# Optimization experiments

Measured on AMD Instinct MI355X. Metric: run time of the kernel, lower is better.

Reference implementation:

```python
import jax, jax.numpy as jnp
import numpy as np

B, T_CHAR, E, N_CHARS, T_TAG = 128, 256, 512, 128, 32


def _rn(k, shape, scale=1.0):
    return jax.random.normal(k, shape, dtype=jnp.float32) * scale


def setup_inputs() -> dict:
    key = jax.random.key(0)
    ks = jax.random.split(key, 24)
    W = 0.05  # param init scale
    tgt_idx = jax.random.randint(ks[4], (B, T_CHAR), 0, N_CHARS)
    return {
        "char_encoding": _rn(ks[0], (B, T_CHAR, E)),
        "char_hn": _rn(ks[1], (2, B, E // 2)),
        "char_cn": _rn(ks[2], (2, B, E // 2)),
        "tag_encoding": _rn(ks[3], (B, T_TAG, E)),
        "true_output_seq": jax.nn.one_hot(tgt_idx, N_CHARS, dtype=jnp.float32),
        # LSTMCell(n_chars -> E), torch gate order i,f,g,o
        "lstm_Wih": _rn(ks[5], (4 * E, N_CHARS), W),
        "lstm_Whh": _rn(ks[6], (4 * E, E), W),
        "lstm_bih": jnp.zeros((4 * E,), jnp.float32),
        "lstm_bhh": jnp.zeros((4 * E,), jnp.float32),
        # char MultiheadAttention (1 head)
        "ca_Wq": _rn(ks[7], (E, E), W), "ca_Wk": _rn(ks[8], (E, E), W), "ca_Wv": _rn(ks[9], (E, E), W),
        "ca_bq": jnp.zeros((E,), jnp.float32), "ca_bk": jnp.zeros((E,), jnp.float32), "ca_bv": jnp.zeros((E,), jnp.float32),
        "ca_Wo": _rn(ks[10], (E, E), W), "ca_bo": jnp.zeros((E,), jnp.float32),
        # tag MultiheadAttention (1 head)
        "ta_Wq": _rn(ks[11], (E, E), W), "ta_Wk": _rn(ks[12], (E, E), W), "ta_Wv": _rn(ks[13], (E, E), W),
        "ta_bq": jnp.zeros((E,), jnp.float32), "ta_bk": jnp.zeros((E,), jnp.float32), "ta_bv": jnp.zeros((E,), jnp.float32),
        "ta_Wo": _rn(ks[14], (E, E), W), "ta_bo": jnp.zeros((E,), jnp.float32),
        # output Linear(2E -> n_chars)
        "out_W": _rn(ks[15], (N_CHARS, 2 * E), W),
        "out_b": jnp.zeros((N_CHARS,), jnp.float32),
    }


def _attend(h, enc_K, enc_V, Wq, bq, Wo, bo):
    # single-head torch MHA: scale query by 1/sqrt(embed_dim)
    q = (h @ Wq.T + bq) * (1.0 / np.sqrt(E))          # [B,E]
    scores = jnp.einsum('be,bse->bs', q, enc_K)        # [B,S]
    a = jax.nn.softmax(scores, axis=-1)
    ctx = jnp.einsum('bs,bse->be', a, enc_V)           # [B,E]
    return ctx @ Wo.T + bo


def reference(char_encoding, char_hn, char_cn, tag_encoding, true_output_seq,
              lstm_Wih, lstm_Whh, lstm_bih, lstm_bhh,
              ca_Wq, ca_Wk, ca_Wv, ca_bq, ca_bk, ca_bv, ca_Wo, ca_bo,
              ta_Wq, ta_Wk, ta_Wv, ta_bq, ta_bk, ta_bv, ta_Wo, ta_bo,
              out_W, out_b):
    # K/V projections are step-invariant: hoist out of the decode loop
    Kc = char_encoding @ ca_Wk.T + ca_bk               # [B,Tc,E]
    Vc = char_encoding @ ca_Wv.T + ca_bv
    Kt = tag_encoding @ ta_Wk.T + ta_bk                # [B,Tt,E]
    Vt = tag_encoding @ ta_Wv.T + ta_bv

    h0 = jnp.concatenate([char_hn[0], char_hn[1]], axis=-1)  # [B,E]
    c0 = jnp.concatenate([char_cn[0], char_cn[1]], axis=-1)

    # teacher forcing: step 0 input is zeros, step t uses true_output_seq[:, t, :]
    x0 = jnp.zeros((char_encoding.shape[0], true_output_seq.shape[-1]), char_encoding.dtype)
    xs = jnp.concatenate([x0[:, None, :], true_output_seq[:, 1:, :]], axis=1)
    xs = jnp.swapaxes(xs, 0, 1)                        # [T,B,n_chars]

    def step(carry, x_t):
        h, c = carry
        gates = x_t @ lstm_Wih.T + lstm_bih + h @ lstm_Whh.T + lstm_bhh
        i, f, g, o = jnp.split(gates, 4, axis=-1)
        c1 = jax.nn.sigmoid(f) * c + jax.nn.sigmoid(i) * jnp.tanh(g)
        h1 = jax.nn.sigmoid(o) * jnp.tanh(c1)
        char_ctx = _attend(h1, Kc, Vc, ca_Wq, ca_bq, ca_Wo, ca_bo)
        tag_ctx = _attend(h1, Kt, Vt, ta_Wq, ta_bq, ta_Wo, ta_bo)
        agg = jax.nn.relu(jnp.concatenate([char_ctx, tag_ctx], axis=-1))  # [B,2E]
        out = agg @ out_W.T + out_b                    # [B,n_chars]
        return (h1, c1), out

    _, outs = jax.lax.scan(step, (h0, c0), xs)         # outs: [T,B,n_chars]
    return jnp.swapaxes(outs, 0, 1)                    # [B,T,n_chars]
```

## Files before the change

kernel.cpp:

```cpp
#include <hip/hip_runtime.h>
#include <cstdint>

#define BB 128
#define TT 256
#define EE 512
#define NC 128
#define STAG 32

#define NWG 64
#define SB 4
#define SC 16
#define NKV 2304

using bf = unsigned short;
typedef __attribute__((ext_vector_type(8))) short short8;
typedef __attribute__((ext_vector_type(8))) unsigned short ushort8;
typedef __attribute__((ext_vector_type(16))) float f32x16;
typedef unsigned long long u64;

static __device__ __forceinline__ float bfu(bf x) { return __uint_as_float(((uint32_t)x) << 16); }
static __device__ __forceinline__ uint32_t f2bf(float f) {
    uint32_t u = __float_as_uint(f);
    return (u + 0x7FFFu + ((u >> 16) & 1u)) >> 16;
}
static __device__ __forceinline__ float sigmoidf_(float x) { return 1.f / (1.f + expf(-x)); }

static __device__ __forceinline__ uint4 pack8bf(float4 a, float4 b) {
    uint4 o;
    o.x = (f2bf(a.y) << 16) | f2bf(a.x);
    o.y = (f2bf(a.w) << 16) | f2bf(a.z);
    o.z = (f2bf(b.y) << 16) | f2bf(b.x);
    o.w = (f2bf(b.w) << 16) | f2bf(b.z);
    return o;
}

static __device__ __forceinline__ uint32_t relu2bf(uint32_t x) {
    uint32_t lo = x & 0xFFFFu, hi = x >> 16;
    lo = (lo & 0x8000u) ? 0u : lo;
    hi = (hi & 0x8000u) ? 0u : hi;
    return lo | (hi << 16);
}

__global__ void diag_ws(float* __restrict__ out, float v, int n) {
    int i = blockIdx.x * 256 + threadIdx.x;
    if (i < n) out[i] = v;
}

__global__ void conv_f2b(const float* __restrict__ s, bf* __restrict__ d, int n) {
    int i = (blockIdx.x * 256 + threadIdx.x) * 4;
    if (i >= n) return;
    float4 v = *(const float4*)(s + i);
    ushort4 o = { (bf)f2bf(v.x), (bf)f2bf(v.y), (bf)f2bf(v.z), (bf)f2bf(v.w) };
    *(ushort4*)(d + i) = o;
}

struct W8 { const float* p[8]; };
__global__ void conv_w8(W8 ws, bf* __restrict__ d) {
    int m = blockIdx.y;
    int i = (blockIdx.x * 256 + threadIdx.x) * 4;
    float4 v = *(const float4*)(ws.p[m] + i);
    ushort4 o = { (bf)f2bf(v.x), (bf)f2bf(v.y), (bf)f2bf(v.z), (bf)f2bf(v.w) };
    *(ushort4*)(d + (size_t)m * 262144 + i) = o;
}

__global__ void h0_pack(const float* __restrict__ hn, bf* __restrict__ Hext) {
    int id = blockIdx.x * 256 + threadIdx.x;
    int b = id >> 9, e = id & 511;
    float v = (e < 256) ? hn[(size_t)b * 256 + e] : hn[(size_t)(BB + b) * 256 + (e - 256)];
    Hext[((size_t)(e >> 3) * BB + b) * 8 + (e & 7)] = (bf)f2bf(v);
}

__global__ void bt_prep2(const float* __restrict__ Whh, bf* __restrict__ Btg2) {
    int id = blockIdx.x * 256 + threadIdx.x;
    int row = id >> 6, chunk = (id & 63) * 8;
    int cg = row >> 7, n = row & 127;
    int r = (n & 3) * 512 + cg * 32 + (n >> 2);
    const float* src = Whh + (size_t)r * 512 + chunk;
    ushort8 o;
#pragma unroll
    for (int i = 0; i < 8; ++i) o[i] = (bf)f2bf(src[i]);
    *(ushort8*)(Btg2 + (size_t)row * 512 + chunk) = o;
}

__global__ void x_prep(const float* __restrict__ tos, int* __restrict__ xidx,
                       float* __restrict__ xval) {
    int id = blockIdx.x * 256 + threadIdx.x;
    int t = id >> 7, b = id & 127;
    int idx = 0; float val = 0.f;
    if (t > 0) {
        const float* row = tos + ((size_t)b * TT + t) * NC;
        for (int k = 0; k < NC; ++k) {
            float v = row[k];
            if (v != 0.f) { idx = k; val = v; }
        }
    }
    xidx[(size_t)t * BB + b] = idx;
    xval[(size_t)t * BB + b] = val;
}

static __device__ __forceinline__ int lds_off(int row, int colbyte) {
    return row * 128 + (colbyte ^ ((row & 7) << 4));
}

template <int MODE>
static __device__ __forceinline__ void worker_gemm(
    const float* __restrict__ Af, const bf* __restrict__ Wb,
    const float* __restrict__ bias, bf* __restrict__ C,
    int bm, int bn, char* smem)
{
    bf* As = (bf*)smem;
    bf* Bs = (bf*)(smem + 16384);
    const int tid = threadIdx.x;
    const int w = tid >> 6, l = tid & 63;
    const int wr = (w >> 1) * 64, wc = (w & 1) * 64;

    f32x16 acc[2][2];
#pragma unroll
    for (int i = 0; i < 2; ++i)
#pragma unroll
        for (int j = 0; j < 2; ++j)
#pragma unroll
            for (int r = 0; r < 16; ++r) acc[i][j][r] = 0.f;

    const int srow = tid >> 3;
    const int scolb = (tid & 7) * 16;
    const int scole = (tid & 7) * 8;

    for (int k0 = 0; k0 < 512; k0 += 64) {
#pragma unroll
        for (int pass = 0; pass < 4; ++pass) {
            int row = pass * 32 + srow;
            const float* ap = Af + (size_t)(bm + row) * 512 + k0 + scole;
            float4 v0 = *(const float4*)ap;
            float4 v1 = *(const float4*)(ap + 4);
            *(uint4*)((char*)As + lds_off(row, scolb)) = pack8bf(v0, v1);
            uint4 vb = *(const uint4*)(Wb + (size_t)(bn + row) * 512 + k0 + scole);
            *(uint4*)((char*)Bs + lds_off(row, scolb)) = vb;
        }
        __syncthreads();
#pragma unroll
        for (int kt = 0; kt < 4; ++kt) {
            const int cb = kt * 32 + (l >> 5) * 16;
            short8 af[2], bfr[2];
#pragma unroll
            for (int i = 0; i < 2; ++i) {
                af[i]  = *(const short8*)((char*)As + lds_off(wr + i * 32 + (l & 31), cb));
                bfr[i] = *(const short8*)((char*)Bs + lds_off(wc + i * 32 + (l & 31), cb));
            }
#pragma unroll
            for (int i = 0; i < 2; ++i)
#pragma unroll
                for (int j = 0; j < 2; ++j)
                    acc[i][j] = __builtin_amdgcn_mfma_f32_32x32x16_bf16(af[i], bfr[j], acc[i][j], 0, 0, 0);
        }
        __syncthreads();
    }

#pragma unroll
    for (int i = 0; i < 2; ++i)
#pragma unroll
        for (int j = 0; j < 2; ++j) {
            int n = bn + wc + j * 32 + (l & 31);
            float bv = bias[n];
#pragma unroll
            for (int r = 0; r < 16; ++r) {
                int m = bm + wr + i * 32 + (r & 3) + 8 * (r >> 2) + 4 * (l >> 5);
                bf v = (bf)f2bf(acc[i][j][r] + bv);
                if constexpr (MODE == 0) {
                    C[(size_t)m * 512 + n] = v;
                } else if constexpr (MODE == 1) {
                    int b = m >> 8, s = m & 255;
                    C[((size_t)b * 512 + n) * 256 + s] = v;
                } else {
                    int b = m >> 5, s = m & 31;
                    C[((size_t)b * 512 + n) * 32 + s] = v;
                }
            }
        }
}

struct KVArgs {
    const float *Ac, *At;
    const bf *WcK, *WcV, *WtK, *WtV;
    const float *bcK, *bcV, *btK, *btV;
    bf *Kc, *VcT, *Kt, *VtT;
};

__global__ __launch_bounds__(256, 1) void lstm_fused(
    bf* __restrict__ Hext,
    const bf* __restrict__ Btg2,
    const float* __restrict__ Wih,
    const float* __restrict__ bih, const float* __restrict__ bhh,
    const float* __restrict__ cn,
    const int* __restrict__ xidx, const float* __restrict__ xval,
    char* __restrict__ flags,
    KVArgs kv)
{
    __shared__ __align__(16) char smem[66048];

    const int gb = blockIdx.x, tid = threadIdx.x;

    if (gb >= NWG) {
        int w = gb - NWG;
        if (w < 1024) {
            worker_gemm<0>(kv.Ac, kv.WcK, kv.bcK, kv.Kc, (w >> 2) * 128, (w & 3) * 128, smem);
        } else if (w < 2048) {
            int t = w - 1024;
            worker_gemm<1>(kv.Ac, kv.WcV, kv.bcV, kv.VcT, (t >> 2) * 128, (t & 3) * 128, smem);
        } else if (w < 2176) {
            int t = w - 2048;
            worker_gemm<0>(kv.At, kv.WtK, kv.btK, kv.Kt, (t >> 2) * 128, (t & 3) * 128, smem);
        } else {
            int t = w - 2176;
            worker_gemm<2>(kv.At, kv.WtV, kv.btV, kv.VtT, (t >> 2) * 128, (t & 3) * 128, smem);
        }
        return;
    }

    bf*    Alds   = (bf*)smem;
    float* gatesf = (float*)smem;
    bf*    wihtp  = (bf*)(smem + 32768);
    float* biass  = (float*)(smem + 65536);

    const int g = gb;
    const int bh = g >> 4, cg = g & 15;

    for (int x = tid; x < 128 * NC; x += 256) {
        int n = x >> 7, k = x & 127;
        int r = (n & 3) * 512 + cg * 32 + (n >> 2);
        wihtp[k * 128 + n] = (bf)f2bf(Wih[(size_t)r * NC + k]);
    }
    if (tid < 128) {
        int r = (tid & 3) * 512 + cg * 32 + (tid >> 2);
        biass[tid] = bih[r] + bhh[r];
    }

    const int b_loc = tid >> 3, u = tid & 7;
    const int b_glob = bh * 32 + b_loc;
    float creg[4];
    {
        int j0 = cg * 32 + u * 4;
        const float* csrc = (cg < 8) ? (cn + (size_t)b_glob * 256 + j0)
                                     : (cn + (size_t)(BB + b_glob) * 256 + (j0 - 256));
#pragma unroll
        for (int i = 0; i < 4; ++i) creg[i] = csrc[i];
    }

    const int wv = tid >> 6, l = tid & 63;

    short8 breg[32];
    {
        const bf* bsrc = Btg2 + ((size_t)(cg * 128 + wv * 32 + (l & 31)) * 512)
                       + (l >> 5) * 8;
#pragma unroll
        for (int kt = 0; kt < 32; ++kt) breg[kt] = *(const short8*)(bsrc + kt * 16);
    }
    __syncthreads();

    const int sb = tid & 31, sg0 = tid >> 5;
    const int dst_lane = sb | ((sg0 & 1) << 5);
    bf* dstbase = Alds + (size_t)(sg0 >> 1) * 512 + dst_lane * 8;

    u64* Hw = (u64*)Hext;
    const size_t SLABB = (size_t)BB * EE * 2;
    const size_t SLAB64 = (size_t)BB * EE / 4;
    const size_t hst_off = (size_t)(cg * 4 + (u >> 1)) * 256 + b_glob * 2 + (u & 1);
    const bf* ards = Alds + l * 8;

    for (int t = 0; t < TT; ++t) {
        const char* At = (const char*)Hext + (size_t)t * SLABB
                       + (size_t)sg0 * 2048 + (size_t)(bh * 32 + sb) * 16;
        uint4 areg[8];
#pragma unroll
        for (int i = 0; i < 8; ++i) {
            asm volatile("global_load_dwordx4 %0, %1, off sc0 sc1"
                         : "=v"(areg[i]) : "v"(At + (size_t)i * 16384));
        }
        float xv = xval[(size_t)t * BB + b_glob];
        int   xi = xidx[(size_t)t * BB + b_glob];
        asm volatile("s_waitcnt vmcnt(0)" ::: "memory");
        __builtin_amdgcn_sched_barrier(0);
#pragma unroll
        for (int i = 0; i < 8; ++i)
            *(uint4*)(dstbase + (size_t)i * 2048) = areg[i];
        __syncthreads();

        f32x16 acc0, acc1;
#pragma unroll
        for (int i = 0; i < 16; ++i) { acc0[i] = 0.f; acc1[i] = 0.f; }
#pragma unroll
        for (int kt = 0; kt < 32; kt += 2) {
            short8 a0 = *(const short8*)(ards + (size_t)kt * 512);
            short8 a1 = *(const short8*)(ards + (size_t)(kt + 1) * 512);
            acc0 = __builtin_amdgcn_mfma_f32_32x32x16_bf16(a0, breg[kt], acc0, 0, 0, 0);
            acc1 = __builtin_amdgcn_mfma_f32_32x32x16_bf16(a1, breg[kt + 1], acc1, 0, 0, 0);
        }
        __syncthreads();
#pragma unroll
        for (int r = 0; r < 16; ++r) {
            int m = (r & 3) + 8 * (r >> 2) + 4 * (l >> 5);
            gatesf[m * 132 + wv * 32 + (l & 31)] = acc0[r] + acc1[r];
        }
        __syncthreads();

        {
            union { ushort4 v; u64 uu; } hout;
#pragma unroll
            for (int i = 0; i < 4; ++i) {
                int nb = (u * 4 + i) * 4;
                float4 ga  = *(const float4*)&gatesf[b_loc * 132 + nb];
                float4 bb4 = *(const float4*)&biass[nb];
                ushort4 xw = *(const ushort4*)&wihtp[xi * 128 + nb];
                float a0 = ga.x + bb4.x + xv * bfu(xw.x);
                float a1 = ga.y + bb4.y + xv * bfu(xw.y);
                float a2 = ga.z + bb4.z + xv * bfu(xw.z);
                float a3 = ga.w + bb4.w + xv * bfu(xw.w);
                float ig = sigmoidf_(a0);
                float fg = sigmoidf_(a1);
                float gg = tanhf(a2);
                float og = sigmoidf_(a3);
                creg[i] = fg * creg[i] + ig * gg;
                float hnew = og * tanhf(creg[i]);
                hout.v[i] = (bf)f2bf(hnew);
            }
            __hip_atomic_store(Hw + (size_t)(t + 1) * SLAB64 + hst_off, hout.uu,
                               __ATOMIC_RELAXED, __HIP_MEMORY_SCOPE_AGENT);
        }

        if (t + 1 < TT) {
            asm volatile("s_waitcnt vmcnt(0)" ::: "memory");
            __syncthreads();
            char* fb = flags + (size_t)(t + 1) * (SB * 2048) + (size_t)bh * 2048;
            if (tid == 0)
                __hip_atomic_store((int*)(fb + (size_t)cg * 128), 1,
                                   __ATOMIC_RELAXED, __HIP_MEMORY_SCOPE_SYSTEM);
            if (tid < 64) {
                const int* fp = (const int*)(fb + (size_t)(tid & 15) * 128);
                while (true) {
                    int v = __hip_atomic_load(fp, __ATOMIC_RELAXED,
                                              __HIP_MEMORY_SCOPE_SYSTEM);
                    if (__all(v != 0)) break;
                    __builtin_amdgcn_s_sleep(1);
                }
            }
            asm volatile("" ::: "memory");
            __syncthreads();
        }
    }
}

template <int S>
static __device__ void attn_side(
    const bf* __restrict__ Hext,
    const bf* __restrict__ Wq, const float* __restrict__ bq,
    const bf* __restrict__ Km,
    const bf* __restrict__ VT,
    const bf* __restrict__ Wo, const float* __restrict__ bo,
    bf* __restrict__ occ,
    int t0, int b, int tid, char* smem)
{
    constexpr int SP = S + 4;
    constexpr int PP = S + 8;
    bf*    Qs   = (bf*)smem;
    float* scs  = (float*)(smem + 33280);
    bf*    Ps   = (bf*)smem;
    bf*    occs = (bf*)(smem + 33280);

    const float QSCALE = 0.044194173824159216f;
    const int wv = tid >> 6, l = tid & 63;
    const int lm = l & 31, lh = l >> 5;

    {
        f32x16 qa[4];
#pragma unroll
        for (int nt = 0; nt < 4; ++nt)
#pragma unroll
            for (int r = 0; r < 16; ++r) qa[nt][r] = 0.f;
#pragma unroll 4
        for (int kt = 0; kt < 32; ++kt) {
            short8 a = *(const short8*)(Hext
                + (((size_t)(t0 + lm + 1) * 64 + kt * 2 + lh) * 1024 + (size_t)b * 8));
#pragma unroll
            for (int nt = 0; nt < 4; ++nt) {
                int n = wv * 128 + nt * 32 + lm;
                short8 w = *(const short8*)(Wq + (size_t)n * 512 + kt * 16 + lh * 8);
                qa[nt] = __builtin_amdgcn_mfma_f32_32x32x16_bf16(a, w, qa[nt], 0, 0, 0);
            }
        }
#pragma unroll
        for (int nt = 0; nt < 4; ++nt) {
            int n = wv * 128 + nt * 32 + lm;
            float bv = bq[n];
#pragma unroll
            for (int r = 0; r < 16; ++r) {
                int m = (r & 3) + 8 * (r >> 2) + 4 * lh;
                Qs[m * 520 + n] = (bf)f2bf((qa[nt][r] + bv) * QSCALE);
            }
        }
    }
    __syncthreads();

    {
        constexpr int NJ = (S == 256) ? 2 : 1;
        f32x16 sa[NJ];
#pragma unroll
        for (int j = 0; j < NJ; ++j)
#pragma unroll
            for (int r = 0; r < 16; ++r) sa[j][r] = 0.f;
#pragma unroll 4
        for (int kt = 0; kt < 32; ++kt) {
            short8 a = *(const short8*)&Qs[lm * 520 + kt * 16 + lh * 8];
#pragma unroll
            for (int j = 0; j < NJ; ++j) {
                int s = ((S == 256) ? (wv * 64 + j * 32) : 0) + lm;
                short8 k8 = *(const short8*)(Km + ((size_t)b * S + s) * 512 + kt * 16 + lh * 8);
                sa[j] = __builtin_amdgcn_mfma_f32_32x32x16_bf16(a, k8, sa[j], 0, 0, 0);
            }
        }
#pragma unroll
        for (int j = 0; j < NJ; ++j) {
            int s = ((S == 256) ? (wv * 64 + j * 32) : 0) + lm;
#pragma unroll
            for (int r = 0; r < 16; ++r) {
                int m = (r & 3) + 8 * (r >> 2) + 4 * lh;
                scs[m * SP + s] = sa[j][r];
            }
        }
    }
    __syncthreads();

    {
        int r = tid >> 3, lg = tid & 7;
        float mx = -1e30f;
        for (int c = lg; c < S; c += 8) mx = fmaxf(mx, scs[r * SP + c]);
#pragma unroll
        for (int d = 1; d < 8; d <<= 1) mx = fmaxf(mx, __shfl_xor(mx, d));
        float sum = 0.f;
        for (int c = lg; c < S; c += 8) {
            float e = expf(scs[r * SP + c] - mx);
            scs[r * SP + c] = e;
            sum += e;
        }
#pragma unroll
        for (int d = 1; d < 8; d <<= 1) sum += __shfl_xor(sum, d);
        float inv = 1.f / sum;
        for (int c = lg; c < S; c += 8) Ps[r * PP + c] = (bf)f2bf(scs[r * SP + c] * inv);
    }
    __syncthreads();

    {
        f32x16 ca[4];
#pragma unroll
        for (int nt = 0; nt < 4; ++nt)
#pragma unroll
            for (int r = 0; r < 16; ++r) ca[nt][r] = 0.f;
#pragma unroll
        for (int kt = 0; kt < S / 16; ++kt) {
            short8 a = *(const short8*)&Ps[lm * PP + kt * 16 + lh * 8];
#pragma unroll
            for (int nt = 0; nt < 4; ++nt) {
                int n = wv * 128 + nt * 32 + lm;
                short8 v8 = *(const short8*)(VT + ((size_t)b * 512 + n) * S + kt * 16 + lh * 8);
                ca[nt] = __builtin_amdgcn_mfma_f32_32x32x16_bf16(a, v8, ca[nt], 0, 0, 0);
            }
        }
        __syncthreads();
#pragma unroll
        for (int nt = 0; nt < 4; ++nt) {
            int n = wv * 128 + nt * 32 + lm;
#pragma unroll
            for (int r = 0; r < 16; ++r) {
                int m = (r & 3) + 8 * (r >> 2) + 4 * lh;
                Qs[m * 520 + n] = (bf)f2bf(ca[nt][r]);
            }
        }
    }
    __syncthreads();

    {
        f32x16 oa[4];
#pragma unroll
        for (int nt = 0; nt < 4; ++nt)
#pragma unroll
            for (int r = 0; r < 16; ++r) oa[nt][r] = 0.f;
#pragma unroll 4
        for (int kt = 0; kt < 32; ++kt) {
            short8 a = *(const short8*)&Qs[lm * 520 + kt * 16 + lh * 8];
#pragma unroll
            for (int nt = 0; nt < 4; ++nt) {
                int n = wv * 128 + nt * 32 + lm;
                short8 w = *(const short8*)(Wo + (size_t)n * 512 + kt * 16 + lh * 8);
                oa[nt] = __builtin_amdgcn_mfma_f32_32x32x16_bf16(a, w, oa[nt], 0, 0, 0);
            }
        }
#pragma unroll
        for (int nt = 0; nt < 4; ++nt) {
            int n = wv * 128 + nt * 32 + lm;
            float bv = bo[n];
#pragma unroll
            for (int r = 0; r < 16; ++r) {
                int m = (r & 3) + 8 * (r >> 2) + 4 * lh;
                occs[m * 520 + n] = (bf)f2bf(oa[nt][r] + bv);
            }
        }
        __syncthreads();
        int row = tid >> 3, c0 = (tid & 7) * 64;
        const bf* src = occs + row * 520 + c0;
        bf* dst = occ + ((size_t)(t0 + row) * BB + b) * 512 + c0;
#pragma unroll
        for (int k = 0; k < 8; ++k)
            *(uint4*)(dst + k * 8) = *(const uint4*)(src + k * 8);
    }
}

struct AttnArgs {
    const bf* Hext;
    const bf *WcQ, *WcO, *WtQ, *WtO;
    const float *bcq, *bco, *btq, *bto;
    const bf *Kc, *VcT, *Kt, *VtT;
    bf *Occ, *Oct;
};

__global__ __launch_bounds__(256, 2) void attn_all(AttnArgs a) {
    __shared__ __align__(16) char smem[66560];
    const int t0 = blockIdx.x * 32, b = blockIdx.y, tid = threadIdx.x;
    if (blockIdx.z == 0)
        attn_side<256>(a.Hext, a.WcQ, a.bcq, a.Kc, a.VcT, a.WcO, a.bco, a.Occ,
                       t0, b, tid, smem);
    else
        attn_side<32>(a.Hext, a.WtQ, a.btq, a.Kt, a.VtT, a.WtO, a.bto, a.Oct,
                      t0, b, tid, smem);
}

__global__ __launch_bounds__(256) void gemm_out(
    const bf* __restrict__ A1, const bf* __restrict__ A2,
    const bf* __restrict__ Wo,
    const float* __restrict__ bias, float* __restrict__ out)
{
    __shared__ __align__(16) bf As[128 * 64];
    __shared__ __align__(16) bf Bs[128 * 64];
    const int tid = threadIdx.x;
    const int bm = blockIdx.x * 128;
    const int w = tid >> 6, l = tid & 63;
    const int wr = (w >> 1) * 64, wc = (w & 1) * 64;

    f32x16 acc[2][2];
#pragma unroll
    for (int i = 0; i < 2; ++i)
#pragma unroll
        for (int j = 0; j < 2; ++j)
#pragma unroll
            for (int r = 0; r < 16; ++r) acc[i][j][r] = 0.f;

    const int srow = tid >> 3;
    const int scolb = (tid & 7) * 16;
    const int scole = (tid & 7) * 8;

    for (int k0 = 0; k0 < 1024; k0 += 64) {
        const bf* Asrc = (k0 < 512) ? A1 : A2;
        const int kk = k0 & 511;
#pragma unroll
        for (int pass = 0; pass < 4; ++pass) {
            int row = pass * 32 + srow;
            uint4 va = *(const uint4*)(Asrc + (size_t)(bm + row) * 512 + kk + scole);
            va.x = relu2bf(va.x); va.y = relu2bf(va.y);
            va.z = relu2bf(va.z); va.w = relu2bf(va.w);
            *(uint4*)((char*)As + lds_off(row, scolb)) = va;
            uint4 vb = *(const uint4*)(Wo + (size_t)row * 1024 + k0 + scole);
            *(uint4*)((char*)Bs + lds_off(row, scolb)) = vb;
        }
        __syncthreads();
#pragma unroll
        for (int kt = 0; kt < 4; ++kt) {
            const int cb = kt * 32 + (l >> 5) * 16;
            short8 af[2], bfr[2];
#pragma unroll
            for (int i = 0; i < 2; ++i) {
                af[i]  = *(const short8*)((char*)As + lds_off(wr + i * 32 + (l & 31), cb));
                bfr[i] = *(const short8*)((char*)Bs + lds_off(wc + i * 32 + (l & 31), cb));
            }
#pragma unroll
            for (int i = 0; i < 2; ++i)
#pragma unroll
                for (int j = 0; j < 2; ++j)
                    acc[i][j] = __builtin_amdgcn_mfma_f32_32x32x16_bf16(af[i], bfr[j], acc[i][j], 0, 0, 0);
        }
        __syncthreads();
    }

#pragma unroll
    for (int i = 0; i < 2; ++i)
#pragma unroll
        for (int j = 0; j < 2; ++j) {
            int n = wc + j * 32 + (l & 31);
            float bv = bias[n];
#pragma unroll
            for (int r = 0; r < 16; ++r) {
                int m = bm + wr + i * 32 + (r & 3) + 8 * (r >> 2) + 4 * (l >> 5);
                int tt = m >> 7, bb_ = m & 127;
                out[((size_t)bb_ * TT + tt) * NC + n] = acc[i][j][r] + bv;
            }
        }
}

extern "C" void kernel_launch(void* const* d_in, const int* in_sizes, int n_in,
                              void* d_out, int out_size, void* d_ws, size_t ws_size,
                              hipStream_t stream) {
    const float* char_enc = (const float*)d_in[0];
    const float* char_hn  = (const float*)d_in[1];
    const float* char_cn  = (const float*)d_in[2];
    const float* tag_enc  = (const float*)d_in[3];
    const float* tos      = (const float*)d_in[4];
    const float* Wih = (const float*)d_in[5];
    const float* Whh = (const float*)d_in[6];
    const float* bih = (const float*)d_in[7];
    const float* bhh = (const float*)d_in[8];
    const float* caWq = (const float*)d_in[9],  *caWk = (const float*)d_in[10], *caWv = (const float*)d_in[11];
    const float* cabq = (const float*)d_in[12], *cabk = (const float*)d_in[13], *cabv = (const float*)d_in[14];
    const float* caWo = (const float*)d_in[15], *cabo = (const float*)d_in[16];
    const float* taWq = (const float*)d_in[17], *taWk = (const float*)d_in[18], *taWv = (const float*)d_in[19];
    const float* tabq = (const float*)d_in[20], *tabk = (const float*)d_in[21], *tabv = (const float*)d_in[22];
    const float* taWo = (const float*)d_in[23], *tabo = (const float*)d_in[24];
    const float* outW = (const float*)d_in[25], *outb = (const float*)d_in[26];
    float* out = (float*)d_out;

    const size_t SZ  = (size_t)TT * BB * EE;
    const size_t SZT = (size_t)BB * STAG * EE;
    const size_t SLAB = (size_t)BB * EE;
    const size_t HEXT = SZ + SLAB;
    const size_t FLAGB = (size_t)TT * SB * 2048;

    const size_t NEED = FLAGB + HEXT * 2 + 4 * SZ * 2 + 2 * SZT * 2
                      + (size_t)SC * 128 * EE * 2 + (size_t)TT * BB * 8
                      + (8 * 262144 + 131072) * 2;
    if (ws_size < NEED) {
        diag_ws<<<dim3((out_size + 255) / 256), dim3(256), 0, stream>>>(
            out, (float)((double)ws_size / 1048576.0), out_size);
        return;
    }

    char* w = (char*)d_ws;
    char* flags = w;             w += FLAGB;
    bf* Hext = (bf*)w;           w += HEXT * 2;
    bf* Kc = (bf*)w;             w += SZ * 2;
    bf* VcT = (bf*)w;            w += SZ * 2;
    bf* Occ = (bf*)w;            w += SZ * 2;
    bf* Oct = (bf*)w;            w += SZ * 2;
    bf* Kt = (bf*)w;             w += SZT * 2;
    bf* VtT = (bf*)w;            w += SZT * 2;
    bf* Btg2 = (bf*)w;           w += (size_t)SC * 128 * EE * 2;
    int* xidx = (int*)w;         w += (size_t)TT * BB * 4;
    float* xval = (float*)w;     w += (size_t)TT * BB * 4;
    bf* Wbf = (bf*)w;            w += 8 * 262144 * 2;
    bf* WoutB = (bf*)w;          w += 131072 * 2;

    bf* WbcaK = Wbf + 0 * 262144; bf* WbcaV = Wbf + 1 * 262144;
    bf* WbcaQ = Wbf + 2 * 262144; bf* WbcaO = Wbf + 3 * 262144;
    bf* WbtaK = Wbf + 4 * 262144; bf* WbtaV = Wbf + 5 * 262144;
    bf* WbtaQ = Wbf + 6 * 262144; bf* WbtaO = Wbf + 7 * 262144;

    hipMemsetAsync(flags, 0, FLAGB, stream);
    h0_pack<<<dim3(256), dim3(256), 0, stream>>>(char_hn, Hext);
    bt_prep2<<<dim3(512), dim3(256), 0, stream>>>(Whh, Btg2);
    x_prep<<<dim3(128), dim3(256), 0, stream>>>(tos, xidx, xval);
    W8 w8; w8.p[0] = caWk; w8.p[1] = caWv; w8.p[2] = caWq; w8.p[3] = caWo;
    w8.p[4] = taWk; w8.p[5] = taWv; w8.p[6] = taWq; w8.p[7] = taWo;
    conv_w8<<<dim3(256, 8), dim3(256), 0, stream>>>(w8, Wbf);
    conv_f2b<<<dim3(128), dim3(256), 0, stream>>>(outW, WoutB, 131072);

    KVArgs kv;
    kv.Ac = char_enc; kv.At = tag_enc;
    kv.WcK = WbcaK; kv.WcV = WbcaV; kv.WtK = WbtaK; kv.WtV = WbtaV;
    kv.bcK = cabk; kv.bcV = cabv; kv.btK = tabk; kv.btV = tabv;
    kv.Kc = Kc; kv.VcT = VcT; kv.Kt = Kt; kv.VtT = VtT;
    lstm_fused<<<dim3(NWG + NKV), dim3(256), 0, stream>>>(
        Hext, Btg2, Wih, bih, bhh, char_cn, xidx, xval, flags, kv);

    AttnArgs aa;
    aa.Hext = Hext;
    aa.WcQ = WbcaQ; aa.WcO = WbcaO; aa.WtQ = WbtaQ; aa.WtO = WbtaO;
    aa.bcq = cabq; aa.bco = cabo; aa.btq = tabq; aa.bto = tabo;
    aa.Kc = Kc; aa.VcT = VcT; aa.Kt = Kt; aa.VtT = VtT;
    aa.Occ = Occ; aa.Oct = Oct;
    attn_all<<<dim3(TT / 32, BB, 2), dim3(256), 0, stream>>>(aa);

    gemm_out<<<dim3(256), dim3(256), 0, stream>>>(Occ, Oct, WoutB, outb, out);
}
```

Before: 1.527 ms.

## Merge prep kernels into one launch and stage H tiles in LDS for Q projection

Replaces the memset and five separate preprocessing kernels with a single prep_all kernel that dispatches work by block index. This cuts per-launch overhead and gaps between small kernels. Separately, the attention Q projection now copies the 32 timesteps of H for its batch row into swizzled LDS before the MFMA loop, instead of issuing strided global loads per k-step. It relies on the flag buffer size matching 512*256*16 bytes and on the LDS region being free at that point.

```diff
diff --git a/kernel.cpp b/kernel.cpp
--- a/kernel.cpp
+++ b/kernel.cpp
@@ -46,56 +46,63 @@
     if (i < n) out[i] = v;
 }
 
-__global__ void conv_f2b(const float* __restrict__ s, bf* __restrict__ d, int n) {
-    int i = (blockIdx.x * 256 + threadIdx.x) * 4;
-    if (i >= n) return;
-    float4 v = *(const float4*)(s + i);
-    ushort4 o = { (bf)f2bf(v.x), (bf)f2bf(v.y), (bf)f2bf(v.z), (bf)f2bf(v.w) };
-    *(ushort4*)(d + i) = o;
-}
-
 struct W8 { const float* p[8]; };
-__global__ void conv_w8(W8 ws, bf* __restrict__ d) {
-    int m = blockIdx.y;
-    int i = (blockIdx.x * 256 + threadIdx.x) * 4;
-    float4 v = *(const float4*)(ws.p[m] + i);
-    ushort4 o = { (bf)f2bf(v.x), (bf)f2bf(v.y), (bf)f2bf(v.z), (bf)f2bf(v.w) };
-    *(ushort4*)(d + (size_t)m * 262144 + i) = o;
-}
-
-__global__ void h0_pack(const float* __restrict__ hn, bf* __restrict__ Hext) {
-    int id = blockIdx.x * 256 + threadIdx.x;
-    int b = id >> 9, e = id & 511;
-    float v = (e < 256) ? hn[(size_t)b * 256 + e] : hn[(size_t)(BB + b) * 256 + (e - 256)];
-    Hext[((size_t)(e >> 3) * BB + b) * 8 + (e & 7)] = (bf)f2bf(v);
-}
-
-__global__ void bt_prep2(const float* __restrict__ Whh, bf* __restrict__ Btg2) {
-    int id = blockIdx.x * 256 + threadIdx.x;
-    int row = id >> 6, chunk = (id & 63) * 8;
-    int cg = row >> 7, n = row & 127;
-    int r = (n & 3) * 512 + cg * 32 + (n >> 2);
-    const float* src = Whh + (size_t)r * 512 + chunk;
-    ushort8 o;
-#pragma unroll
-    for (int i = 0; i < 8; ++i) o[i] = (bf)f2bf(src[i]);
-    *(ushort8*)(Btg2 + (size_t)row * 512 + chunk) = o;
-}
-
-__global__ void x_prep(const float* __restrict__ tos, int* __restrict__ xidx,
-                       float* __restrict__ xval) {
-    int id = blockIdx.x * 256 + threadIdx.x;
-    int t = id >> 7, b = id & 127;
-    int idx = 0; float val = 0.f;
-    if (t > 0) {
-        const float* row = tos + ((size_t)b * TT + t) * NC;
-        for (int k = 0; k < NC; ++k) {
-            float v = row[k];
-            if (v != 0.f) { idx = k; val = v; }
-        }
-    }
-    xidx[(size_t)t * BB + b] = idx;
-    xval[(size_t)t * BB + b] = val;
+struct PrepArgs {
+    char* flags;
+    const float* hn; bf* Hext;
+    const float* Whh; bf* Btg2;
+    const float* tos; int* xidx; float* xval;
+    W8 w8; bf* Wbf;
+    const float* outW; bf* WoutB;
+};
+
+__global__ __launch_bounds__(256) void prep_all(PrepArgs p) {
+    const int blk = blockIdx.x, tid = threadIdx.x;
+    if (blk < 512) {
+        uint4 z = {0u, 0u, 0u, 0u};
+        ((uint4*)p.flags)[blk * 256 + tid] = z;
+    } else if (blk < 768) {
+        int id = (blk - 512) * 256 + tid;
+        int b = id >> 9, e = id & 511;
+        float v = (e < 256) ? p.hn[(size_t)b * 256 + e]
+                            : p.hn[(size_t)(BB + b) * 256 + (e - 256)];
+        p.Hext[((size_t)(e >> 3) * BB + b) * 8 + (e & 7)] = (bf)f2bf(v);
+    } else if (blk < 1280) {
+        int id = (blk - 768) * 256 + tid;
+        int row = id >> 6, chunk = (id & 63) * 8;
+        int cg = row >> 7, n = row & 127;
+        int r = (n & 3) * 512 + cg * 32 + (n >> 2);
+        const float* src = p.Whh + (size_t)r * 512 + chunk;
+        ushort8 o;
+#pragma unroll
+        for (int i = 0; i < 8; ++i) o[i] = (bf)f2bf(src[i]);
+        *(ushort8*)(p.Btg2 + (size_t)row * 512 + chunk) = o;
+    } else if (blk < 1408) {
+        int id = (blk - 1280) * 256 + tid;
+        int t = id >> 7, b = id & 127;
+        int idx = 0; float val = 0.f;
+        if (t > 0) {
+            const float* row = p.tos + ((size_t)b * TT + t) * NC;
+            for (int k = 0; k < NC; ++k) {
+                float v = row[k];
+                if (v != 0.f) { idx = k; val = v; }
+            }
+        }
+        p.xidx[(size_t)t * BB + b] = idx;
+        p.xval[(size_t)t * BB + b] = val;
+    } else if (blk < 3456) {
+        int idx = blk - 1408;
+        int m = idx >> 8;
+        int i = ((idx & 255) * 256 + tid) * 4;
+        float4 v = *(const float4*)(p.w8.p[m] + i);
+        ushort4 o = { (bf)f2bf(v.x), (bf)f2bf(v.y), (bf)f2bf(v.z), (bf)f2bf(v.w) };
+        *(ushort4*)(p.Wbf + (size_t)m * 262144 + i) = o;
+    } else {
+        int i = ((blk - 3456) * 256 + tid) * 4;
+        float4 v = *(const float4*)(p.outW + i);
+        ushort4 o = { (bf)f2bf(v.x), (bf)f2bf(v.y), (bf)f2bf(v.z), (bf)f2bf(v.w) };
+        *(ushort4*)(p.WoutB + i) = o;
+    }
 }
 
 static __device__ __forceinline__ int lds_off(int row, int colbyte) {
@@ -365,11 +372,19 @@
     float* scs  = (float*)(smem + 33280);
     bf*    Ps   = (bf*)smem;
     bf*    occs = (bf*)(smem + 33280);
+    char*  Hs   = smem + 33280;
 
     const float QSCALE = 0.044194173824159216f;
     const int wv = tid >> 6, l = tid & 63;
     const int lm = l & 31, lh = l >> 5;
 
+    for (int x = tid; x < 2048; x += 256) {
+        int tl = x >> 6, grp = x & 63;
+        uint4 v = *(const uint4*)(Hext + (((size_t)(t0 + tl + 1) * 64 + grp) * BB + b) * 8);
+        *(uint4*)(Hs + tl * 1024 + ((grp ^ (tl & 7)) << 4)) = v;
+    }
+    __syncthreads();
+
     {
         f32x16 qa[4];
 #pragma unroll
@@ -378,8 +393,7 @@
             for (int r = 0; r < 16; ++r) qa[nt][r] = 0.f;
 #pragma unroll 4
         for (int kt = 0; kt < 32; ++kt) {
-            short8 a = *(const short8*)(Hext
-                + (((size_t)(t0 + lm + 1) * 64 + kt * 2 + lh) * 1024 + (size_t)b * 8));
+            short8 a = *(const short8*)(Hs + lm * 1024 + (((kt * 2 + lh) ^ (lm & 7)) << 4));
 #pragma unroll
             for (int nt = 0; nt < 4; ++nt) {
                 int n = wv * 128 + nt * 32 + lm;
@@ -659,14 +673,16 @@
     bf* WbtaK = Wbf + 4 * 262144; bf* WbtaV = Wbf + 5 * 262144;
     bf* WbtaQ = Wbf + 6 * 262144; bf* WbtaO = Wbf + 7 * 262144;
 
-    hipMemsetAsync(flags, 0, FLAGB, stream);
-    h0_pack<<<dim3(256), dim3(256), 0, stream>>>(char_hn, Hext);
-    bt_prep2<<<dim3(512), dim3(256), 0, stream>>>(Whh, Btg2);
-    x_prep<<<dim3(128), dim3(256), 0, stream>>>(tos, xidx, xval);
-    W8 w8; w8.p[0] = caWk; w8.p[1] = caWv; w8.p[2] = caWq; w8.p[3] = caWo;
-    w8.p[4] = taWk; w8.p[5] = taWv; w8.p[6] = taWq; w8.p[7] = taWo;
-    conv_w8<<<dim3(256, 8), dim3(256), 0, stream>>>(w8, Wbf);
-    conv_f2b<<<dim3(128), dim3(256), 0, stream>>>(outW, WoutB, 131072);
+    PrepArgs pp;
+    pp.flags = flags;
+    pp.hn = char_hn; pp.Hext = Hext;
+    pp.Whh = Whh; pp.Btg2 = Btg2;
+    pp.tos = tos; pp.xidx = xidx; pp.xval = xval;
+    pp.w8.p[0] = caWk; pp.w8.p[1] = caWv; pp.w8.p[2] = caWq; pp.w8.p[3] = caWo;
+    pp.w8.p[4] = taWk; pp.w8.p[5] = taWv; pp.w8.p[6] = taWq; pp.w8.p[7] = taWo;
+    pp.Wbf = Wbf;
+    pp.outW = outW; pp.WoutB = WoutB;
+    prep_all<<<dim3(3584), dim3(256), 0, stream>>>(pp);
 
     KVArgs kv;
     kv.Ac = char_enc; kv.At = tag_enc;
```

Result: faster. 1.473 ms (median of 2 runs) (-3.5%).
